# Kernel tuning notes

Hardware: AMD Instinct MI355X
Metric: run time of the kernel (lower is better)

The kernel has to match this reference:

```python
import jax, jax.numpy as jnp
import numpy as np

B, N, DIM, H, DH, PD = 2, 1024, 768, 8, 64, 4
EPS = 1e-8


def setup_inputs() -> dict:
    key = jax.random.key(0)
    ks = jax.random.split(key, 12)
    w = lambda k, shp: jax.random.normal(k, shp, dtype=jnp.float32) * 0.02
    return {
        "x": jax.random.normal(ks[0], (B, N, DIM), dtype=jnp.float32),
        "rotations": jax.random.normal(ks[1], (B, N, 3, 3), dtype=jnp.float32),
        "translations": jax.random.normal(ks[2], (B, N, 3), dtype=jnp.float32),
        "W_sq": w(ks[3], (H * DH, DIM)),
        "W_sk": w(ks[4], (H * DH, DIM)),
        "W_sv": w(ks[5], (H * DH, DIM)),
        "W_pq": w(ks[6], (H * PD * 3, DIM)),
        "W_pk": w(ks[7], (H * PD * 3, DIM)),
        "W_pv": w(ks[8], (H * PD * 3, DIM)),
        "point_weights": jax.random.normal(ks[9], (H,), dtype=jnp.float32),
        "W_out": w(ks[10], (DIM, H * (DH + PD * 4))),
        "b_out": jax.random.normal(ks[11], (DIM,), dtype=jnp.float32) * 0.02,
    }


def reference(x, rotations, translations, W_sq, W_sk, W_sv, W_pq, W_pk, W_pv, point_weights, W_out, b_out):
    b, n, _ = x.shape
    h, dh, pd = H, DH, PD
    scalar_scale = (2 * dh) ** -0.5           # num_attn_logits=2
    point_scale = (2 * pd * (9 / 2)) ** -0.5

    # scalar q/k/v: [b,h,n,dh]
    qs = (x @ W_sq.T).reshape(b, n, h, dh).transpose(0, 2, 1, 3)
    ks = (x @ W_sk.T).reshape(b, n, h, dh).transpose(0, 2, 1, 3)
    vs = (x @ W_sv.T).reshape(b, n, h, dh).transpose(0, 2, 1, 3)

    # point q/k/v: [b,h,n,pd,3]
    qp = (x @ W_pq.T).reshape(b, n, h, pd, 3).transpose(0, 2, 1, 3, 4)
    kp = (x @ W_pk.T).reshape(b, n, h, pd, 3).transpose(0, 2, 1, 3, 4)
    vp = (x @ W_pv.T).reshape(b, n, h, pd, 3).transpose(0, 2, 1, 3, 4)

    t = translations[:, None, :, None, :]  # [b,1,n,1,3]
    # global-frame points: p_c = sum_r R[n,c,r] * p[d,r] + t
    qp = jnp.einsum('bncr,bhndr->bhndc', rotations, qp) + t
    kp = jnp.einsum('bncr,bhndr->bhndc', rotations, kp) + t
    vp = jnp.einsum('bncr,bhndr->bhndc', rotations, vp) + t

    # scalar attention logits [b,h,i,j]
    logits = jnp.einsum('bhid,bhjd->bhij', qs, ks) * scalar_scale

    # point distance term: sum_{d,c} (q-k)^2 = |q|^2 + |k|^2 - 2 q.k (no [i,j,d,c] tensor)
    q2 = jnp.sum(qp ** 2, axis=(-1, -2))  # [b,h,i]
    k2 = jnp.sum(kp ** 2, axis=(-1, -2))  # [b,h,j]
    qk = jnp.einsum('bhidc,bhjdc->bhij', qp, kp)
    point_dist = q2[..., :, None] + k2[..., None, :] - 2.0 * qk

    pw = jax.nn.softplus(point_weights)[None, :, None, None]  # [1,h,1,1]
    logits = logits - 0.5 * (point_dist * pw * point_scale)

    attn = jax.nn.softmax(logits, axis=-1)

    rs = jnp.einsum('bhij,bhjd->bhid', attn, vs)          # [b,h,n,dh]
    rp = jnp.einsum('bhij,bhjdc->bhidc', attn, vp)        # [b,h,n,pd,3]
    # back to local frame: R^T (p - t)
    rp = jnp.einsum('bnrc,bhndr->bhndc', rotations, rp - t)
    rn = jnp.sqrt(jnp.sum(rp ** 2, axis=-1) + EPS)        # [b,h,n,pd]

    rs = rs.transpose(0, 2, 1, 3).reshape(b, n, h * dh)
    rp_f = rp.transpose(0, 2, 1, 3, 4).reshape(b, n, h * pd * 3)
    rn = rn.transpose(0, 2, 1, 3).reshape(b, n, h * pd)

    results = jnp.concatenate([rs, rp_f, rn], axis=-1)    # [b,n,640]
    return results @ W_out.T + b_out
```

## Files before the change

### kernel.cpp

```cpp
#include <hip/hip_runtime.h>
#include <hip/hip_bf16.h>
#include <math.h>

#define B_  2
#define N_  1024
#define DIM_ 768
#define H_  8
#define DH_ 64
#define PD_ 4
#define NPROJ 1824
#define NPAD  1920
#define BH_ (B_*H_)
#define FDIM 640

#define OFF_RS   0u
#define OFF_RP   (OFF_RS + (size_t)BH_*N_*DH_)
#define OFF_PRAW (OFF_RP + (size_t)BH_*N_*12)
#define OFF_QA   (OFF_PRAW + (size_t)B_*N_*288)
#define OFF_KA   (OFF_QA + (size_t)BH_*N_*96/2)
#define OFF_VT   (OFF_KA + (size_t)BH_*N_*96/2)
#define OFF_XB   (OFF_VT + (size_t)BH_*80*N_/2)
#define OFF_WB   (OFF_XB + (size_t)B_*N_*DIM_/2)
#define OFF_FB   OFF_XB
#define OFF_WOB  OFF_WB

typedef __attribute__((ext_vector_type(8))) short bf16x8;
typedef __attribute__((ext_vector_type(4))) float f32x4;

__device__ __forceinline__ float dot4(float4 a, float4 b) {
    return a.x*b.x + a.y*b.y + a.z*b.z + a.w*b.w;
}
__device__ __forceinline__ unsigned short f2bf(float f) {
    __hip_bfloat16 h = __float2bfloat16(f);
    return *reinterpret_cast<unsigned short*>(&h);
}

__global__ __launch_bounds__(256) void k_cvt_x(
    const float* __restrict__ x, unsigned short* __restrict__ xb)
{
    int i = blockIdx.x * 256 + threadIdx.x;
    if (i >= (B_*N_*DIM_)/4) return;
    float4 v = reinterpret_cast<const float4*>(x)[i];
    ushort4 o;
    o.x = f2bf(v.x); o.y = f2bf(v.y); o.z = f2bf(v.z); o.w = f2bf(v.w);
    reinterpret_cast<ushort4*>(xb)[i] = o;
}

__global__ __launch_bounds__(256) void k_cvt_w(
    const float* __restrict__ Wsq, const float* __restrict__ Wsk,
    const float* __restrict__ Wsv, const float* __restrict__ Wpq,
    const float* __restrict__ Wpk, const float* __restrict__ Wpv,
    unsigned short* __restrict__ wb)
{
    int i = blockIdx.x * 256 + threadIdx.x;
    if (i >= (NPAD*DIM_)/4) return;
    int row = i / (DIM_/4);
    int c4  = i % (DIM_/4);
    ushort4 o;
    if (row >= NPROJ) {
        o.x = o.y = o.z = o.w = 0;
    } else {
        const float* W;
        if      (row < 512)  W = Wsq + (size_t)row*DIM_;
        else if (row < 1024) W = Wsk + (size_t)(row-512)*DIM_;
        else if (row < 1536) W = Wsv + (size_t)(row-1024)*DIM_;
        else if (row < 1632) W = Wpq + (size_t)(row-1536)*DIM_;
        else if (row < 1728) W = Wpk + (size_t)(row-1632)*DIM_;
        else                 W = Wpv + (size_t)(row-1728)*DIM_;
        float4 v = reinterpret_cast<const float4*>(W)[c4];
        o.x = f2bf(v.x); o.y = f2bf(v.y); o.z = f2bf(v.z); o.w = f2bf(v.w);
    }
    reinterpret_cast<ushort4*>(wb)[i] = o;
}

__global__ __launch_bounds__(256) void k_cvt_wout(
    const float* __restrict__ Wout, unsigned short* __restrict__ wob)
{
    int i = blockIdx.x * 256 + threadIdx.x;
    if (i >= (DIM_*FDIM)/4) return;
    float4 v = reinterpret_cast<const float4*>(Wout)[i];
    ushort4 o;
    o.x = f2bf(v.x); o.y = f2bf(v.y); o.z = f2bf(v.z); o.w = f2bf(v.w);
    reinterpret_cast<ushort4*>(wob)[i] = o;
}

__global__ __launch_bounds__(256) void k_proj_mfma(
    const unsigned short* __restrict__ xb,
    const unsigned short* __restrict__ wb,
    float* __restrict__ ws)
{
    __shared__ unsigned short sAB[2*128*32];
    const int tid  = threadIdx.x;
    const int lane = tid & 63;
    const int wid  = tid >> 6;
    const int mt = blockIdx.x & 15;
    const int nt = blockIdx.x >> 4;
    const int row0 = mt*128;
    const int col0 = nt*128;
    const int wr = (wid >> 1)*64;
    const int wc = (wid & 1)*64;

    f32x4 acc[4][4];
    #pragma unroll
    for (int m = 0; m < 4; ++m)
        #pragma unroll
        for (int n = 0; n < 4; ++n) acc[m][n] = (f32x4){0.f,0.f,0.f,0.f};

    for (int kt = 0; kt < DIM_/32; ++kt) {
        __syncthreads();
        #pragma unroll
        for (int t = 0; t < 4; ++t) {
            int chunk = t*4 + wid;
            int tile  = chunk >> 3;
            int crow  = (chunk & 7) * 16;
            int grow  = (tile ? col0 : row0) + crow + (lane >> 2);
            const unsigned short* gsrc = (tile ? wb : xb)
                + (size_t)grow*DIM_ + kt*32 + (lane & 3)*8;
            __builtin_amdgcn_global_load_lds(
                (const __attribute__((address_space(1))) void*)gsrc,
                (__attribute__((address_space(3))) void*)(sAB + chunk*512),
                16, 0, 0);
        }
        __syncthreads();

        bf16x8 a[4], b[4];
        #pragma unroll
        for (int m = 0; m < 4; ++m)
            a[m] = *reinterpret_cast<const bf16x8*>(
                sAB + ((wr + m*16 + (lane & 15))*32 + (lane >> 4)*8));
        #pragma unroll
        for (int n = 0; n < 4; ++n)
            b[n] = *reinterpret_cast<const bf16x8*>(
                sAB + 128*32 + ((wc + n*16 + (lane & 15))*32 + (lane >> 4)*8));
        #pragma unroll
        for (int m = 0; m < 4; ++m)
            #pragma unroll
            for (int n = 0; n < 4; ++n)
                acc[m][n] = __builtin_amdgcn_mfma_f32_16x16x32_bf16(
                    a[m], b[n], acc[m][n], 0, 0, 0);
    }

    unsigned short* qa = (unsigned short*)(ws + OFF_QA);
    unsigned short* ka = (unsigned short*)(ws + OFF_KA);
    unsigned short* vt = (unsigned short*)(ws + OFF_VT);
    float* praw = ws + OFF_PRAW;
    const float ss = 0.08838834764831845f;

    #pragma unroll
    for (int n = 0; n < 4; ++n) {
        int o = col0 + wc + n*16 + (lane & 15);
        if (o >= NPROJ) continue;
        #pragma unroll
        for (int m = 0; m < 4; ++m) {
            #pragma unroll
            for (int j = 0; j < 4; ++j) {
                int r = row0 + wr + m*16 + (lane >> 4)*4 + j;
                int bb = r >> 10, nn = r & (N_-1);
                float v = acc[m][n][j];
                if (o < 512) {
                    int h = o >> 6, c = o & 63;
                    qa[((size_t)(bb*H_ + h)*N_ + nn)*96 + c] = f2bf(v*ss);
                } else if (o < 1024) {
                    int oo = o - 512; int h = oo >> 6, c = oo & 63;
                    ka[((size_t)(bb*H_ + h)*N_ + nn)*96 + c] = f2bf(v);
                } else if (o < 1536) {
                    int oo = o - 1024; int h = oo >> 6, c = oo & 63;
                    vt[((size_t)(bb*H_ + h)*80 + c)*N_ + nn] = f2bf(v);
                } else {
                    praw[(size_t)r*288 + (o - 1536)] = v;
                }
            }
        }
    }
}

__global__ __launch_bounds__(128) void k_prep(
    const float* __restrict__ rot_g,
    const float* __restrict__ trans_g,
    const float* __restrict__ pw_g,
    float* __restrict__ ws)
{
    __shared__ float R[9], T[3];
    __shared__ float rot[3][8][4][3];
    __shared__ float p2[2][8][4];
    __shared__ float q2t[8], k2t[8], coefs[8];
    const int tid = threadIdx.x;
    const int row = blockIdx.x;
    const int b = row >> 10, n = row & (N_-1);

    if (tid < 9)  R[tid] = rot_g[(size_t)row*9 + tid];
    if (tid >= 9 && tid < 12) T[tid-9] = trans_g[(size_t)row*3 + (tid-9)];
    if (tid >= 16 && tid < 24) {
        float pw = pw_g[tid-16];
        coefs[tid-16] = 0.5f * log1pf(__expf(pw)) * (1.0f/6.0f);
    }
    __syncthreads();
    if (tid < 96) {
        int which = tid >> 5, idx = tid & 31;
        int h = idx >> 2, pd = idx & 3;
        const float* p = ws + OFF_PRAW + (size_t)row*288 + which*96 + h*12 + pd*3;
        float px = p[0], py = p[1], pz = p[2];
        float c0 = R[0]*px + R[1]*py + R[2]*pz + T[0];
        float c1 = R[3]*px + R[4]*py + R[5]*pz + T[1];
        float c2 = R[6]*px + R[7]*py + R[8]*pz + T[2];
        rot[which][h][pd][0] = c0;
        rot[which][h][pd][1] = c1;
        rot[which][h][pd][2] = c2;
        if (which < 2) p2[which][h][pd] = c0*c0 + c1*c1 + c2*c2;
    }
    __syncthreads();
    if (tid < 16) {
        int w = tid >> 3, h = tid & 7;
        float s = p2[w][h][0] + p2[w][h][1] + p2[w][h][2] + p2[w][h][3];
        if (w) k2t[h] = s; else q2t[h] = s;
    }
    __syncthreads();

    unsigned short* qa = (unsigned short*)(ws + OFF_QA);
    unsigned short* ka = (unsigned short*)(ws + OFF_KA);
    unsigned short* vt = (unsigned short*)(ws + OFF_VT);

    for (int i = tid; i < 256; i += 128) {
        int h = i >> 5, c = i & 31;
        float qv, kv;
        if (c < 12)      { qv = rot[0][h][c/3][c%3] * 2.f * coefs[h]; kv = rot[1][h][c/3][c%3]; }
        else if (c == 12){ qv = q2t[h];  kv = -coefs[h]; }
        else if (c == 13){ qv = 1.f;     kv = -coefs[h]*k2t[h]; }
        else             { qv = 0.f;     kv = 0.f; }
        size_t base = ((size_t)(b*H_ + h)*N_ + n)*96 + 64 + c;
        qa[base] = f2bf(qv);
        ka[base] = f2bf(kv);
    }
    {
        int h = tid >> 4, r = tid & 15;
        float vv = (r < 12) ? rot[2][h][r/3][r%3] : 0.f;
        vt[((size_t)(b*H_ + h)*80 + 64 + r)*N_ + n] = f2bf(vv);
    }
}

#define KPAD 104
#define VPAD 72
__global__ __launch_bounds__(256) void k_attn_mfma(
    const unsigned short* __restrict__ qa_g,
    const unsigned short* __restrict__ ka_g,
    const unsigned short* __restrict__ vt_g,
    float* __restrict__ ws)
{
    __shared__ unsigned short sKa[2][64*KPAD];
    __shared__ unsigned short sVt[2][80*VPAD];
    __shared__ unsigned short sP[4][16*VPAD];
    __shared__ float sMrg[32*80];
    __shared__ float sML[32*2];

    const int tid  = threadIdx.x;
    const int lane = tid & 63;
    const int wid  = tid >> 6;
    const int bh = blockIdx.x >> 5;
    const int qt = blockIdx.x & 31;
    const int q0 = qt * 32;
    const int mrow = (wid & 1) * 16;
    const int half = wid >> 1;
    const int tg   = tid & 127;

    const unsigned short* Qa = qa_g + (size_t)bh*N_*96;
    const unsigned short* Ka = ka_g + (size_t)bh*N_*96;
    const unsigned short* Vt = vt_g + (size_t)bh*80*N_;

    bf16x8 qfr[3];
    {
        int qrow = q0 + mrow + (lane & 15);
        #pragma unroll
        for (int c = 0; c < 3; ++c)
            qfr[c] = *reinterpret_cast<const bf16x8*>(
                Qa + (size_t)qrow*96 + c*32 + (lane >> 4)*8);
    }

    f32x4 acc[5];
    #pragma unroll
    for (int d = 0; d < 5; ++d) acc[d] = (f32x4){0.f,0.f,0.f,0.f};
    float m[4] = {-1e30f,-1e30f,-1e30f,-1e30f};
    float l[4] = {0.f,0.f,0.f,0.f};

    for (int it = 0; it < 8; ++it) {
        const int j0 = (half*8 + it)*64;
        __syncthreads();
        for (int i = tg; i < 768; i += 128) {
            int r = i / 12, c = i % 12;
            *reinterpret_cast<uint4*>(&sKa[half][r*KPAD + c*8]) =
                *reinterpret_cast<const uint4*>(Ka + (size_t)(j0+r)*96 + c*8);
        }
        for (int i = tg; i < 640; i += 128) {
            int r = i >> 3, c = i & 7;
            *reinterpret_cast<uint4*>(&sVt[half][r*VPAD + c*8]) =
                *reinterpret_cast<const uint4*>(Vt + (size_t)r*N_ + j0 + c*8);
        }
        __syncthreads();

        f32x4 s[4];
        #pragma unroll
        for (int t = 0; t < 4; ++t) s[t] = (f32x4){0.f,0.f,0.f,0.f};
        #pragma unroll
        for (int c = 0; c < 3; ++c) {
            #pragma unroll
            for (int t = 0; t < 4; ++t) {
                bf16x8 kb = *reinterpret_cast<const bf16x8*>(
                    &sKa[half][(t*16 + (lane & 15))*KPAD + c*32 + (lane >> 4)*8]);
                s[t] = __builtin_amdgcn_mfma_f32_16x16x32_bf16(qfr[c], kb, s[t], 0, 0, 0);
            }
        }

        float scl[4];
        #pragma unroll
        for (int r = 0; r < 4; ++r) {
            float v = fmaxf(fmaxf(s[0][r], s[1][r]), fmaxf(s[2][r], s[3][r]));
            v = fmaxf(v, __shfl_xor(v, 1));
            v = fmaxf(v, __shfl_xor(v, 2));
            v = fmaxf(v, __shfl_xor(v, 4));
            v = fmaxf(v, __shfl_xor(v, 8));
            float mn = fmaxf(m[r], v);
            scl[r] = __expf(m[r] - mn);
            m[r] = mn;
        }
        float ps[4] = {0.f,0.f,0.f,0.f};
        #pragma unroll
        for (int t = 0; t < 4; ++t) {
            #pragma unroll
            for (int r = 0; r < 4; ++r) {
                float p = __expf(s[t][r] - m[r]);
                ps[r] += p;
                sP[wid][((lane >> 4)*4 + r)*VPAD + t*16 + (lane & 15)] = f2bf(p);
            }
        }
        #pragma unroll
        for (int r = 0; r < 4; ++r) {
            float v = ps[r];
            v += __shfl_xor(v, 1);
            v += __shfl_xor(v, 2);
            v += __shfl_xor(v, 4);
            v += __shfl_xor(v, 8);
            l[r] = l[r]*scl[r] + v;
        }
        #pragma unroll
        for (int d = 0; d < 5; ++d)
            #pragma unroll
            for (int r = 0; r < 4; ++r) acc[d][r] *= scl[r];

        #pragma unroll
        for (int kk = 0; kk < 2; ++kk) {
            bf16x8 pa = *reinterpret_cast<const bf16x8*>(
                &sP[wid][(lane & 15)*VPAD + kk*32 + (lane >> 4)*8]);
            #pragma unroll
            for (int dt = 0; dt < 5; ++dt) {
                bf16x8 vb = *reinterpret_cast<const bf16x8*>(
                    &sVt[half][(dt*16 + (lane & 15))*VPAD + kk*32 + (lane >> 4)*8]);
                acc[dt] = __builtin_amdgcn_mfma_f32_16x16x32_bf16(pa, vb, acc[dt], 0, 0, 0);
            }
        }
    }

    __syncthreads();
    if (half == 1) {
        #pragma unroll
        for (int r = 0; r < 4; ++r) {
            int rl = mrow + (lane >> 4)*4 + r;
            #pragma unroll
            for (int dt = 0; dt < 5; ++dt)
                sMrg[rl*80 + dt*16 + (lane & 15)] = acc[dt][r];
            if ((lane & 15) == 0) { sML[rl*2] = m[r]; sML[rl*2+1] = l[r]; }
        }
    }
    __syncthreads();
    if (half == 0) {
        float* ws_rs = ws + OFF_RS + (size_t)bh*N_*DH_;
        float* ws_rp = ws + OFF_RP + (size_t)bh*N_*12;
        #pragma unroll
        for (int r = 0; r < 4; ++r) {
            int rl = mrow + (lane >> 4)*4 + r;
            float m2 = sML[rl*2], l2 = sML[rl*2+1];
            float mm = fmaxf(m[r], m2);
            float f1 = __expf(m[r] - mm), f2 = __expf(m2 - mm);
            float inv = 1.f / (l[r]*f1 + l2*f2);
            int i = q0 + rl;
            #pragma unroll
            for (int dt = 0; dt < 5; ++dt) {
                float val = (acc[dt][r]*f1 + sMrg[rl*80 + dt*16 + (lane & 15)]*f2) * inv;
                int d = dt*16 + (lane & 15);
                if (d < 64)
                    ws_rs[(size_t)i*DH_ + d] = val;
                else if (d - 64 < 12)
                    ws_rp[(size_t)i*12 + (d - 64)] = val;
            }
        }
    }
}

__global__ __launch_bounds__(256) void k_fin_prep(
    const float* __restrict__ rotations,
    const float* __restrict__ translations,
    const float* __restrict__ ws,
    unsigned short* __restrict__ fb)
{
    __shared__ float sF[8][FDIM];
    const int tid = threadIdx.x;
    const int row0 = blockIdx.x * 8;
    const int b = row0 >> 10;
    const float* ws_rs = ws + OFF_RS;
    const float* ws_rp = ws + OFF_RP;

    for (int i = tid; i < 8*512; i += 256) {
        int r = i >> 9, f = i & 511;
        int h = f >> 6, c = f & 63;
        int n = (row0 & (N_-1)) + r;
        sF[r][f] = ws_rs[(((size_t)(b*H_ + h))*N_ + n)*DH_ + c];
    }
    {
        int r = tid >> 5;
        int idx = tid & 31;
        int h = idx >> 2, pd = idx & 3;
        int row = row0 + r;
        int n = row & (N_-1);
        const float* rp = ws_rp + (((size_t)(b*H_ + h))*N_ + n)*12 + pd*3;
        const float* R = rotations + (size_t)row*9;
        const float* T = translations + (size_t)row*3;
        float d0 = rp[0] - T[0], d1 = rp[1] - T[1], d2 = rp[2] - T[2];
        float l0 = R[0]*d0 + R[3]*d1 + R[6]*d2;
        float l1 = R[1]*d0 + R[4]*d1 + R[7]*d2;
        float l2 = R[2]*d0 + R[5]*d1 + R[8]*d2;
        sF[r][512 + h*12 + pd*3 + 0] = l0;
        sF[r][512 + h*12 + pd*3 + 1] = l1;
        sF[r][512 + h*12 + pd*3 + 2] = l2;
        sF[r][608 + h*4 + pd] = sqrtf(l0*l0 + l1*l1 + l2*l2 + 1e-8f);
    }
    __syncthreads();

    #pragma unroll
    for (int r = 0; r < 8; ++r) {
        for (int f = tid; f < FDIM; f += 256) {
            fb[(size_t)(row0 + r)*FDIM + f] = f2bf(sF[r][f]);
        }
    }
}

__global__ __launch_bounds__(256) void k_out_mfma(
    const unsigned short* __restrict__ fb,
    const unsigned short* __restrict__ wob,
    const float* __restrict__ bout,
    float* __restrict__ out)
{
    __shared__ unsigned short sAB[2*128*32];
    const int tid  = threadIdx.x;
    const int lane = tid & 63;
    const int wid  = tid >> 6;
    const int mt = blockIdx.x & 15;
    const int nt = blockIdx.x >> 4;
    const int row0 = mt*128;
    const int col0 = nt*128;
    const int wr = (wid >> 1)*64;
    const int wc = (wid & 1)*64;

    f32x4 acc[4][4];
    #pragma unroll
    for (int m = 0; m < 4; ++m)
        #pragma unroll
        for (int n = 0; n < 4; ++n) acc[m][n] = (f32x4){0.f,0.f,0.f,0.f};

    for (int kt = 0; kt < FDIM/32; ++kt) {
        __syncthreads();
        #pragma unroll
        for (int t = 0; t < 4; ++t) {
            int chunk = t*4 + wid;
            int tile  = chunk >> 3;
            int crow  = (chunk & 7) * 16;
            int grow  = (tile ? col0 : row0) + crow + (lane >> 2);
            const unsigned short* gsrc = (tile ? wob : fb)
                + (size_t)grow*FDIM + kt*32 + (lane & 3)*8;
            __builtin_amdgcn_global_load_lds(
                (const __attribute__((address_space(1))) void*)gsrc,
                (__attribute__((address_space(3))) void*)(sAB + chunk*512),
                16, 0, 0);
        }
        __syncthreads();

        bf16x8 a[4], b[4];
        #pragma unroll
        for (int m = 0; m < 4; ++m)
            a[m] = *reinterpret_cast<const bf16x8*>(
                sAB + ((wr + m*16 + (lane & 15))*32 + (lane >> 4)*8));
        #pragma unroll
        for (int n = 0; n < 4; ++n)
            b[n] = *reinterpret_cast<const bf16x8*>(
                sAB + 128*32 + ((wc + n*16 + (lane & 15))*32 + (lane >> 4)*8));
        #pragma unroll
        for (int m = 0; m < 4; ++m)
            #pragma unroll
            for (int n = 0; n < 4; ++n)
                acc[m][n] = __builtin_amdgcn_mfma_f32_16x16x32_bf16(
                    a[m], b[n], acc[m][n], 0, 0, 0);
    }

    #pragma unroll
    for (int n = 0; n < 4; ++n) {
        int o = col0 + wc + n*16 + (lane & 15);
        float bo = bout[o];
        #pragma unroll
        for (int m = 0; m < 4; ++m) {
            #pragma unroll
            for (int j = 0; j < 4; ++j) {
                int r = row0 + wr + m*16 + (lane >> 4)*4 + j;
                out[(size_t)r*DIM_ + o] = acc[m][n][j] + bo;
            }
        }
    }
}

extern "C" void kernel_launch(void* const* d_in, const int* in_sizes, int n_in,
                              void* d_out, int out_size, void* d_ws, size_t ws_size,
                              hipStream_t stream) {
    const float* x            = (const float*)d_in[0];
    const float* rotations    = (const float*)d_in[1];
    const float* translations = (const float*)d_in[2];
    const float* Wsq          = (const float*)d_in[3];
    const float* Wsk          = (const float*)d_in[4];
    const float* Wsv          = (const float*)d_in[5];
    const float* Wpq          = (const float*)d_in[6];
    const float* Wpk          = (const float*)d_in[7];
    const float* Wpv          = (const float*)d_in[8];
    const float* pweights     = (const float*)d_in[9];
    const float* Wout         = (const float*)d_in[10];
    const float* bout         = (const float*)d_in[11];
    float* out = (float*)d_out;
    float* ws  = (float*)d_ws;

    unsigned short* xb  = (unsigned short*)(ws + OFF_XB);
    unsigned short* wb  = (unsigned short*)(ws + OFF_WB);
    unsigned short* qa  = (unsigned short*)(ws + OFF_QA);
    unsigned short* ka  = (unsigned short*)(ws + OFF_KA);
    unsigned short* vt  = (unsigned short*)(ws + OFF_VT);
    unsigned short* fb  = (unsigned short*)(ws + OFF_FB);
    unsigned short* wob = (unsigned short*)(ws + OFF_WOB);

    k_cvt_x<<<(B_*N_*DIM_/4 + 255)/256, 256, 0, stream>>>(x, xb);
    k_cvt_w<<<(NPAD*DIM_/4 + 255)/256, 256, 0, stream>>>(Wsq, Wsk, Wsv, Wpq, Wpk, Wpv, wb);
    k_proj_mfma<<<16*15, 256, 0, stream>>>(xb, wb, ws);
    k_prep<<<B_*N_, 128, 0, stream>>>(rotations, translations, pweights, ws);
    k_attn_mfma<<<BH_*32, 256, 0, stream>>>(qa, ka, vt, ws);
    k_cvt_wout<<<(DIM_*FDIM/4 + 255)/256, 256, 0, stream>>>(Wout, wob);
    k_fin_prep<<<B_*N_/8, 256, 0, stream>>>(rotations, translations, ws, fb);
    k_out_mfma<<<16*6, 256, 0, stream>>>(fb, wob, bout, out);
}
```

Measured before the change: 108.8 us.

## Load K and V MFMA fragments directly from global memory, dropping LDS staging

The attention kernel no longer stages K and V^T tiles through shared memory. Each wave now reads its MFMA B-operand fragments straight from global memory, relying on L1/L2 for reuse across the two waves in each half. This removes the two __syncthreads per tile iteration and the LDS store/load round trip, and frees LDS so more blocks can be resident. The cost is redundant global loads, since both waves in a half fetch the same K/V rows, and loads issued immediately before the MFMAs with no prefetching.

```diff
diff --git a/kernel.cpp b/kernel.cpp
--- a/kernel.cpp
+++ b/kernel.cpp
@@ -238,7 +238,6 @@
     }
 }
 
-#define KPAD 104
 #define VPAD 72
 __global__ __launch_bounds__(256) void k_attn_mfma(
     const unsigned short* __restrict__ qa_g,
@@ -246,8 +245,6 @@
     const unsigned short* __restrict__ vt_g,
     float* __restrict__ ws)
 {
-    __shared__ unsigned short sKa[2][64*KPAD];
-    __shared__ unsigned short sVt[2][80*VPAD];
     __shared__ unsigned short sP[4][16*VPAD];
     __shared__ float sMrg[32*80];
     __shared__ float sML[32*2];
@@ -255,12 +252,13 @@
     const int tid  = threadIdx.x;
     const int lane = tid & 63;
     const int wid  = tid >> 6;
+    const int lo = lane & 15;
+    const int hi = lane >> 4;
     const int bh = blockIdx.x >> 5;
     const int qt = blockIdx.x & 31;
     const int q0 = qt * 32;
     const int mrow = (wid & 1) * 16;
     const int half = wid >> 1;
-    const int tg   = tid & 127;
 
     const unsigned short* Qa = qa_g + (size_t)bh*N_*96;
     const unsigned short* Ka = ka_g + (size_t)bh*N_*96;
@@ -268,11 +266,11 @@
 
     bf16x8 qfr[3];
     {
-        int qrow = q0 + mrow + (lane & 15);
+        int qrow = q0 + mrow + lo;
         #pragma unroll
         for (int c = 0; c < 3; ++c)
             qfr[c] = *reinterpret_cast<const bf16x8*>(
-                Qa + (size_t)qrow*96 + c*32 + (lane >> 4)*8);
+                Qa + (size_t)qrow*96 + c*32 + hi*8);
     }
 
     f32x4 acc[5];
@@ -283,30 +281,20 @@
 
     for (int it = 0; it < 8; ++it) {
         const int j0 = (half*8 + it)*64;
-        __syncthreads();
-        for (int i = tg; i < 768; i += 128) {
-            int r = i / 12, c = i % 12;
-            *reinterpret_cast<uint4*>(&sKa[half][r*KPAD + c*8]) =
-                *reinterpret_cast<const uint4*>(Ka + (size_t)(j0+r)*96 + c*8);
-        }
-        for (int i = tg; i < 640; i += 128) {
-            int r = i >> 3, c = i & 7;
-            *reinterpret_cast<uint4*>(&sVt[half][r*VPAD + c*8]) =
-                *reinterpret_cast<const uint4*>(Vt + (size_t)r*N_ + j0 + c*8);
-        }
-        __syncthreads();
 
         f32x4 s[4];
         #pragma unroll
         for (int t = 0; t < 4; ++t) s[t] = (f32x4){0.f,0.f,0.f,0.f};
         #pragma unroll
         for (int c = 0; c < 3; ++c) {
-            #pragma unroll
-            for (int t = 0; t < 4; ++t) {
-                bf16x8 kb = *reinterpret_cast<const bf16x8*>(
-                    &sKa[half][(t*16 + (lane & 15))*KPAD + c*32 + (lane >> 4)*8]);
-                s[t] = __builtin_amdgcn_mfma_f32_16x16x32_bf16(qfr[c], kb, s[t], 0, 0, 0);
-            }
+            bf16x8 kb[4];
+            #pragma unroll
+            for (int t = 0; t < 4; ++t)
+                kb[t] = *reinterpret_cast<const bf16x8*>(
+                    Ka + (size_t)(j0 + t*16 + lo)*96 + c*32 + hi*8);
+            #pragma unroll
+            for (int t = 0; t < 4; ++t)
+                s[t] = __builtin_amdgcn_mfma_f32_16x16x32_bf16(qfr[c], kb[t], s[t], 0, 0, 0);
         }
 
         float scl[4];
@@ -328,7 +316,7 @@
             for (int r = 0; r < 4; ++r) {
                 float p = __expf(s[t][r] - m[r]);
                 ps[r] += p;
-                sP[wid][((lane >> 4)*4 + r)*VPAD + t*16 + (lane & 15)] = f2bf(p);
+                sP[wid][(hi*4 + r)*VPAD + t*16 + lo] = f2bf(p);
             }
         }
         #pragma unroll
@@ -348,11 +336,11 @@
         #pragma unroll
         for (int kk = 0; kk < 2; ++kk) {
             bf16x8 pa = *reinterpret_cast<const bf16x8*>(
-                &sP[wid][(lane & 15)*VPAD + kk*32 + (lane >> 4)*8]);
+                &sP[wid][lo*VPAD + kk*32 + hi*8]);
             #pragma unroll
             for (int dt = 0; dt < 5; ++dt) {
                 bf16x8 vb = *reinterpret_cast<const bf16x8*>(
-                    &sVt[half][(dt*16 + (lane & 15))*VPAD + kk*32 + (lane >> 4)*8]);
+                    Vt + (size_t)(dt*16 + lo)*N_ + j0 + kk*32 + hi*8);
                 acc[dt] = __builtin_amdgcn_mfma_f32_16x16x32_bf16(pa, vb, acc[dt], 0, 0, 0);
             }
         }
@@ -362,11 +350,11 @@
     if (half == 1) {
         #pragma unroll
         for (int r = 0; r < 4; ++r) {
-            int rl = mrow + (lane >> 4)*4 + r;
+            int rl = mrow + hi*4 + r;
             #pragma unroll
             for (int dt = 0; dt < 5; ++dt)
-                sMrg[rl*80 + dt*16 + (lane & 15)] = acc[dt][r];
-            if ((lane & 15) == 0) { sML[rl*2] = m[r]; sML[rl*2+1] = l[r]; }
+                sMrg[rl*80 + dt*16 + lo] = acc[dt][r];
+            if (lo == 0) { sML[rl*2] = m[r]; sML[rl*2+1] = l[r]; }
         }
     }
     __syncthreads();
@@ -375,7 +363,7 @@
         float* ws_rp = ws + OFF_RP + (size_t)bh*N_*12;
         #pragma unroll
         for (int r = 0; r < 4; ++r) {
-            int rl = mrow + (lane >> 4)*4 + r;
+            int rl = mrow + hi*4 + r;
             float m2 = sML[rl*2], l2 = sML[rl*2+1];
             float mm = fmaxf(m[r], m2);
             float f1 = __expf(m[r] - mm), f2 = __expf(m2 - mm);
@@ -383,8 +371,8 @@
             int i = q0 + rl;
             #pragma unroll
             for (int dt = 0; dt < 5; ++dt) {
-                float val = (acc[dt][r]*f1 + sMrg[rl*80 + dt*16 + (lane & 15)]*f2) * inv;
-                int d = dt*16 + (lane & 15);
+                float val = (acc[dt][r]*f1 + sMrg[rl*80 + dt*16 + lo]*f2) * inv;
+                int d = dt*16 + lo;
                 if (d < 64)
                     ws_rs[(size_t)i*DH_ + d] = val;
                 else if (d - 64 < 12)
```

Result: slower. 112.7 us (+3.6%).
